# Kernel tuning notes

Measured on AMD Instinct MI355X. Metric: run time of the kernel, lower is better.

Reference implementation:

```python
import jax, jax.numpy as jnp
import numpy as np

B, NP, NM, C, H = 4, 256, 128, 128, 128
EPS = 1e-5

def layernorm(x, g, b):
    mu = jnp.mean(x, axis=-1, keepdims=True)
    var = jnp.var(x, axis=-1, keepdims=True)
    return (x - mu) * jax.lax.rsqrt(var + EPS) * g + b

def setup_inputs() -> dict:
    key = jax.random.key(0)
    ks = jax.random.split(key, 16)
    s = lambda d: 1.0 / np.sqrt(d)
    return {
        "z": jax.random.normal(ks[0], (B, NP, NM, C), jnp.float32),
        "z_mask": jnp.ones((B, NP, NM), jnp.float32),
        "pocket_pair": jax.random.normal(ks[1], (B, NP, NP, C), jnp.float32),
        "mol_pair": jax.random.normal(ks[2], (B, NM, NM, C), jnp.float32),
        "ln_g": jnp.ones((C,), jnp.float32), "ln_b": jnp.zeros((C,), jnp.float32),
        "lnh_g": jnp.ones((H,), jnp.float32), "lnh_b": jnp.zeros((H,), jnp.float32),
        "gw1": jax.random.uniform(ks[3], (C, H), jnp.float32, -s(C), s(C)),
        "gb1": jnp.zeros((H,), jnp.float32),
        "gw2": jax.random.uniform(ks[4], (C, H), jnp.float32, -s(C), s(C)),
        "gb2": jnp.zeros((H,), jnp.float32),
        "w1": jax.random.uniform(ks[5], (C, H), jnp.float32, -s(C), s(C)),
        "b1": jnp.zeros((H,), jnp.float32),
        "w2": jax.random.uniform(ks[6], (C, H), jnp.float32, -s(C), s(C)),
        "b2": jnp.zeros((H,), jnp.float32),
        "egw": jax.random.uniform(ks[7], (C, C), jnp.float32, -s(C), s(C)),
        "egb": jnp.zeros((C,), jnp.float32),
        "asw": jax.random.uniform(ks[8], (H, C), jnp.float32, -s(H), s(H)),
        "asb": jnp.zeros((C,), jnp.float32),
    }

def reference(z, z_mask, pocket_pair, mol_pair, ln_g, ln_b, lnh_g, lnh_b,
              gw1, gb1, gw2, gb2, w1, b1, w2, b2, egw, egb, asw, asb):
    m = z_mask[..., None]                      # [b,Np,Nm,1]
    zn = layernorm(z, ln_g, ln_b)              # [b,Np,Nm,C]
    pp = layernorm(pocket_pair, ln_g, ln_b)    # [b,Np,Np,C]
    mp = layernorm(mol_pair, ln_g, ln_b)       # [b,Nm,Nm,C]
    gate1 = lambda x: jax.nn.sigmoid(x @ gw1 + gb1) * (x @ w1 + b1)
    gate2 = lambda x: jax.nn.sigmoid(x @ gw2 + gb2) * (x @ w2 + b2)
    ab1 = gate1(zn) * m                        # [b,Np,Nm,H]
    ab2 = gate2(zn) * m                        # [b,Np,Nm,H]
    ppg = gate2(pp)                            # [b,Np,Np,H]
    mpg = gate1(mp)                            # [b,Nm,Nm,H]
    block1 = jnp.einsum('bikc,bkjc->bijc', ppg, ab1)   # [b,Np,Nm,H]
    block2 = jnp.einsum('bikc,bjkc->bijc', ab2, mpg)   # [b,Np,Nm,H]
    h = layernorm(block1 + block2, lnh_g, lnh_b)
    out = jax.nn.sigmoid(zn @ egw + egb) * (h @ asw + asb) * m
    return out
```

## Files before the change

kernel.cpp:

```cpp
#include <hip/hip_runtime.h>
#include <hip/hip_bf16.h>

#define DEVFN __device__ __forceinline__
using bf16 = __hip_bfloat16;
typedef __attribute__((ext_vector_type(8))) short short8;
typedef __attribute__((ext_vector_type(4))) float f32x4;
typedef __attribute__((ext_vector_type(4))) unsigned short us4;

constexpr int BB = 4, NP = 256, NM = 128, CC = 128, HH = 128;
constexpr float EPS = 1e-5f;

#define MFMA16(a,b,c) __builtin_amdgcn_mfma_f32_16x16x32_bf16((a),(b),(c),0,0,0)

DEVFN unsigned short bfbits(float v){ union{ bf16 b; unsigned short s; } u; u.b = __float2bfloat16(v); return u.s; }
DEVFN float bits2f(unsigned short s){ union{ unsigned int i; float f; } u; u.i = ((unsigned)s) << 16; return u.f; }
DEVFN float sigm(float x){ return 1.0f / (1.0f + __expf(-x)); }

__global__ __launch_bounds__(256)
void prep_weights_kernel(const float* __restrict__ gw1, const float* __restrict__ w1,
                         const float* __restrict__ gw2, const float* __restrict__ w2,
                         const float* __restrict__ egw, const float* __restrict__ asw,
                         bf16* __restrict__ wt)
{
  __shared__ float wl[128][129];
  const int bx = blockIdx.x;
  const float* W = (bx==0)?gw1 : (bx==1)?w1 : (bx==2)?gw2 : (bx==3)?w2 : (bx==4)?egw : asw;
  const int t = threadIdx.x;
  for (int i = 0; i < 16; ++i){
    int idx = t + 256*i;
    int k = idx >> 5, n0 = (idx & 31) * 4;
    float4 v = *reinterpret_cast<const float4*>(W + k*128 + n0);
    wl[k][n0] = v.x; wl[k][n0+1] = v.y; wl[k][n0+2] = v.z; wl[k][n0+3] = v.w;
  }
  __syncthreads();
  short* o = reinterpret_cast<short*>(wt) + bx * 16384;
  const int n = t >> 1, kh = t & 1;
  #pragma unroll
  for (int j = 0; j < 8; ++j){
    short8 p;
    #pragma unroll
    for (int u = 0; u < 8; ++u) p[u] = (short)bfbits(wl[kh*64 + j*8 + u][n]);
    *reinterpret_cast<short8*>(o + n*128 + kh*64 + j*8) = p;
  }
}

struct GateSmem {
  short xs[64*128];
  float lgb[2][128];
  float mk[64];
};

DEVFN void gate_pass64(const char* xb, const float* mk, int t, long obase, long R,
                       const short* wtg, const short* wtl,
                       const float* __restrict__ bgp, const float* __restrict__ blp,
                       bf16* outp)
{
  const int l = t & 63, w = t >> 6, lr = l & 15, lg = l >> 4;
  const int n0 = w * 32;
  short8 bgf[2][4], blf[2][4];
  #pragma unroll
  for (int nt = 0; nt < 2; ++nt)
    #pragma unroll
    for (int ks = 0; ks < 4; ++ks){
      int n = n0 + nt*16 + lr, ko = ks*32 + lg*8;
      bgf[nt][ks] = *reinterpret_cast<const short8*>(wtg + n*128 + ko);
      blf[nt][ks] = *reinterpret_cast<const short8*>(wtl + n*128 + ko);
    }
  float bgv[2] = { bgp[n0 + lr], bgp[n0 + 16 + lr] };
  float blv[2] = { blp[n0 + lr], blp[n0 + 16 + lr] };
  unsigned short* ob = reinterpret_cast<unsigned short*>(outp);

  #pragma unroll
  for (int mt = 0; mt < 4; ++mt){
    f32x4 zv = {0.f,0.f,0.f,0.f};
    f32x4 ag0 = zv, ag1 = zv, al0 = zv, al1 = zv;
    #pragma unroll
    for (int ks = 0; ks < 4; ++ks){
      int m = mt*16 + lr, ko = ks*32 + lg*8;
      short8 a = *reinterpret_cast<const short8*>(xb + ((m*256 + ko*2) ^ ((m & 7) << 4)));
      ag0 = MFMA16(a, bgf[0][ks], ag0);
      al0 = MFMA16(a, blf[0][ks], al0);
      ag1 = MFMA16(a, bgf[1][ks], ag1);
      al1 = MFMA16(a, blf[1][ks], al1);
    }
    #pragma unroll
    for (int nt = 0; nt < 2; ++nt){
      f32x4 ag = nt ? ag1 : ag0, al = nt ? al1 : al0;
      int h = n0 + nt*16 + lr;
      us4 pk;
      #pragma unroll
      for (int rg = 0; rg < 4; ++rg){
        int rowl = mt*16 + lg*4 + rg;
        float val = sigm(ag[rg] + bgv[nt]) * (al[rg] + blv[nt]) * mk[rowl];
        pk[rg] = bfbits(val);
      }
      *reinterpret_cast<us4*>(ob + obase + (long)h*R + mt*16 + lg*4) = pk;
    }
  }
}

DEVFN void eg_pass64(const char* xb, int t, long obase, long R,
                     const short* wtg, const float* __restrict__ bgp, bf16* outp)
{
  const int l = t & 63, w = t >> 6, lr = l & 15, lg = l >> 4;
  const int n0 = w * 32;
  short8 bgf[2][4];
  #pragma unroll
  for (int nt = 0; nt < 2; ++nt)
    #pragma unroll
    for (int ks = 0; ks < 4; ++ks){
      int n = n0 + nt*16 + lr, ko = ks*32 + lg*8;
      bgf[nt][ks] = *reinterpret_cast<const short8*>(wtg + n*128 + ko);
    }
  float bgv[2] = { bgp[n0 + lr], bgp[n0 + 16 + lr] };
  unsigned short* ob = reinterpret_cast<unsigned short*>(outp);

  #pragma unroll
  for (int mt = 0; mt < 4; ++mt){
    f32x4 zv = {0.f,0.f,0.f,0.f};
    f32x4 ag0 = zv, ag1 = zv;
    #pragma unroll
    for (int ks = 0; ks < 4; ++ks){
      int m = mt*16 + lr, ko = ks*32 + lg*8;
      short8 a = *reinterpret_cast<const short8*>(xb + ((m*256 + ko*2) ^ ((m & 7) << 4)));
      ag0 = MFMA16(a, bgf[0][ks], ag0);
      ag1 = MFMA16(a, bgf[1][ks], ag1);
    }
    #pragma unroll
    for (int nt = 0; nt < 2; ++nt){
      f32x4 ag = nt ? ag1 : ag0;
      int h = n0 + nt*16 + lr;
      us4 pk;
      #pragma unroll
      for (int rg = 0; rg < 4; ++rg) pk[rg] = bfbits(sigm(ag[rg] + bgv[nt]));
      *reinterpret_cast<us4*>(ob + obase + (long)h*R + mt*16 + lg*4) = pk;
    }
  }
}

constexpr int NZB = (BB*NP*NM)/64;
constexpr int NPB = (BB*NP*NP)/64;
constexpr int NMB = (BB*NM*NM)/64;

__global__ __launch_bounds__(256, 3)
void gate_all_kernel(const float* __restrict__ z, const float* __restrict__ zmask,
                     const float* __restrict__ pp, const float* __restrict__ mp,
                     const float* __restrict__ lng, const float* __restrict__ lnb,
                     const bf16* __restrict__ wt,
                     const float* __restrict__ gb1, const float* __restrict__ b1,
                     const float* __restrict__ gb2, const float* __restrict__ b2,
                     const float* __restrict__ egbv,
                     bf16* ab1, bf16* ab2, bf16* egp, bf16* ppg, bf16* mpg)
{
  __shared__ GateSmem sm;
  const int t = threadIdx.x;
  const short* wts = reinterpret_cast<const short*>(wt);

  int bx = blockIdx.x;
  const float* x; const float* mask = nullptr;
  long R; int npass = 1;
  const short *w1g, *w1l; const float *bg1v, *bl1v; bf16* o1;
  if (bx < NZB){
    x = z; mask = zmask; R = (long)NP*NM; npass = 3;
    w1g = wts + 0*16384; w1l = wts + 1*16384; bg1v = gb1; bl1v = b1; o1 = ab1;
  } else if (bx < NZB + NPB){
    bx -= NZB; x = pp; R = (long)NP*NP;
    w1g = wts + 2*16384; w1l = wts + 3*16384; bg1v = gb2; bl1v = b2; o1 = ppg;
  } else {
    bx -= NZB + NPB; x = mp; R = (long)NM*NM;
    w1g = wts + 0*16384; w1l = wts + 1*16384; bg1v = gb1; bl1v = b1; o1 = mpg;
  }
  const long row0 = (long)bx * 64;
  const int b = (int)(row0 / R);
  const long rowb = row0 - (long)b * R;
  const long obase = (long)b * 128 * R + rowb;

  if (t < 128){ sm.lgb[0][t] = lng[t]; sm.lgb[1][t] = lnb[t]; }
  if (t < 64) sm.mk[t] = mask ? mask[row0 + t] : 1.0f;

  const int r = t >> 2, hf = t & 3;
  const float4* xrow = reinterpret_cast<const float4*>(x + (row0 + r)*128 + hf*32);
  float4 vb[8];
  float s = 0.f, ss = 0.f;
  #pragma unroll
  for (int i = 0; i < 8; ++i){
    float4 v = xrow[i]; vb[i] = v;
    s  += v.x + v.y + v.z + v.w;
    ss += v.x*v.x + v.y*v.y + v.z*v.z + v.w*v.w;
  }
  s += __shfl_xor(s, 1);  ss += __shfl_xor(ss, 1);
  s += __shfl_xor(s, 2);  ss += __shfl_xor(ss, 2);
  const float mu = s * (1.f/128.f);
  const float rsg = rsqrtf(ss * (1.f/128.f) - mu*mu + EPS);
  __syncthreads();
  {
    char* xb = reinterpret_cast<char*>(sm.xs);
    #pragma unroll
    for (int j = 0; j < 4; ++j){
      float4 a = vb[2*j], c2 = vb[2*j+1];
      float vv[8] = {a.x, a.y, a.z, a.w, c2.x, c2.y, c2.z, c2.w};
      short8 p;
      #pragma unroll
      for (int u = 0; u < 8; ++u){
        int ch = hf*32 + j*8 + u;
        p[u] = (short)bfbits((vv[u] - mu) * rsg * sm.lgb[0][ch] + sm.lgb[1][ch]);
      }
      *reinterpret_cast<short8*>(xb + ((r*256 + hf*64 + j*16) ^ ((r & 7) << 4))) = p;
    }
  }
  __syncthreads();

  const char* xb = reinterpret_cast<const char*>(sm.xs);
  gate_pass64(xb, sm.mk, t, obase, R, w1g, w1l, bg1v, bl1v, o1);
  if (npass == 3){
    gate_pass64(xb, sm.mk, t, obase, R, wts + 2*16384, wts + 3*16384, gb2, b2, ab2);
    eg_pass64(xb, t, obase, R, wts + 4*16384, egbv, egp);
  }
}

DEVFN int b1swz(int j){ return (((j & 7) ^ ((j >> 3) & 7)) << 4); }

__global__ __launch_bounds__(256, 2)
void einsum_mfma_kernel(const bf16* __restrict__ ppg, const bf16* __restrict__ ab1,
                        const bf16* __restrict__ ab2, const bf16* __restrict__ mpg,
                        bf16* __restrict__ bsum)
{
  __shared__ short b1t[128*256];
  const int t = threadIdx.x, l = t & 63, w = t >> 6, lr = l & 15, lg = l >> 4;
  const int bc = blockIdx.x;
  const short* A1 = reinterpret_cast<const short*>(ppg) + (long)bc * (NP*NP);
  const short* B1 = reinterpret_cast<const short*>(ab1) + (long)bc * (NP*NM);
  const short* A2 = reinterpret_cast<const short*>(ab2) + (long)bc * (NP*NM);
  const short* B2 = reinterpret_cast<const short*>(mpg) + (long)bc * (NM*NM);

  char* lb = reinterpret_cast<char*>(b1t);
  for (int it = 0; it < 16; ++it){
    int idx = t + 256*it;
    int k = idx >> 4, j0 = (idx & 15) * 8;
    short8 v = *reinterpret_cast<const short8*>(B1 + idx*8);
    #pragma unroll
    for (int u = 0; u < 8; ++u){
      int j = j0 + u;
      *reinterpret_cast<short*>(lb + ((j*512 + k*2) ^ b1swz(j))) = v[u];
    }
  }
  __syncthreads();

  f32x4 zv = {0.f,0.f,0.f,0.f};
  f32x4 acc[4][8];
  #pragma unroll
  for (int i = 0; i < 4; ++i)
    #pragma unroll
    for (int j = 0; j < 8; ++j) acc[i][j] = zv;

  const int m0 = w * 64;
  for (int ks = 0; ks < 8; ++ks){
    int ko = ks*32 + lg*8;
    short8 af[4];
    #pragma unroll
    for (int mt = 0; mt < 4; ++mt)
      af[mt] = *reinterpret_cast<const short8*>(A1 + (m0 + mt*16 + lr)*256 + ko);
    short8 bf[8];
    #pragma unroll
    for (int nt = 0; nt < 8; ++nt){
      int n = nt*16 + lr;
      bf[nt] = *reinterpret_cast<const short8*>(lb + ((n*512 + ko*2) ^ b1swz(n)));
    }
    #pragma unroll
    for (int mt = 0; mt < 4; ++mt)
      #pragma unroll
      for (int nt = 0; nt < 8; ++nt)
        acc[mt][nt] = MFMA16(af[mt], bf[nt], acc[mt][nt]);
  }
  for (int ks = 0; ks < 4; ++ks){
    int ko = ks*32 + lg*8;
    short8 af[4];
    #pragma unroll
    for (int mt = 0; mt < 4; ++mt)
      af[mt] = *reinterpret_cast<const short8*>(A2 + (m0 + mt*16 + lr)*128 + ko);
    short8 bf[8];
    #pragma unroll
    for (int nt = 0; nt < 8; ++nt)
      bf[nt] = *reinterpret_cast<const short8*>(B2 + (nt*16 + lr)*128 + ko);
    #pragma unroll
    for (int mt = 0; mt < 4; ++mt)
      #pragma unroll
      for (int nt = 0; nt < 8; ++nt)
        acc[mt][nt] = MFMA16(af[mt], bf[nt], acc[mt][nt]);
  }
  unsigned short* out = reinterpret_cast<unsigned short*>(bsum) + (long)bc * (NP*NM);
  #pragma unroll
  for (int mt = 0; mt < 4; ++mt)
    #pragma unroll
    for (int nt = 0; nt < 8; ++nt)
      #pragma unroll
      for (int rg = 0; rg < 4; ++rg)
        out[(m0 + mt*16 + lg*4 + rg)*128 + nt*16 + lr] = bfbits(acc[mt][nt][rg]);
}

__global__ __launch_bounds__(256, 2)
void final_mfma_kernel(const bf16* __restrict__ bsum, const bf16* __restrict__ eg,
                       const float* __restrict__ mask,
                       const float* __restrict__ lnhg, const float* __restrict__ lnhb,
                       const bf16* __restrict__ wt, const float* __restrict__ asb,
                       float* __restrict__ out)
{
  __shared__ struct {
    short xsT[128][72];
    short xs[64*128];
    float lgb[2][128];
    float ps[4][64], pss[4][64];
    float mu[64], rs[64], mk[64];
  } sm;
  const int t = threadIdx.x, l = t & 63, w = t >> 6, lr = l & 15, lg = l >> 4;
  const long row0 = (long)blockIdx.x * 64;
  const int b = (int)(row0 >> 15);
  const long rowb = row0 & 32767;

  if (t < 128){ sm.lgb[0][t] = lnhg[t]; sm.lgb[1][t] = lnhb[t]; }
  if (t < 64) sm.mk[t] = mask[row0 + t];

  const short* bs = reinterpret_cast<const short*>(bsum);
  #pragma unroll
  for (int i = 0; i < 4; ++i){
    int idx = t + 256*i;
    int c = idx >> 3, j8 = idx & 7;
    short8 v = *reinterpret_cast<const short8*>(bs + (long)(b*128 + c)*32768 + rowb + j8*8);
    *reinterpret_cast<short8*>(&sm.xsT[c][j8*8]) = v;
  }
  __syncthreads();
  {
    int ij = t & 63, q = t >> 6;
    float s = 0.f, ss = 0.f;
    #pragma unroll
    for (int k = 0; k < 32; ++k){
      float v = bits2f((unsigned short)sm.xsT[q*32 + k][ij]);
      s += v; ss += v*v;
    }
    sm.ps[q][ij] = s; sm.pss[q][ij] = ss;
  }
  __syncthreads();
  if (t < 64){
    float s  = sm.ps[0][t] + sm.ps[1][t] + sm.ps[2][t] + sm.ps[3][t];
    float ss = sm.pss[0][t] + sm.pss[1][t] + sm.pss[2][t] + sm.pss[3][t];
    float mu = s * (1.f/128.f);
    float var = ss * (1.f/128.f) - mu*mu;
    sm.mu[t] = mu; sm.rs[t] = rsqrtf(var + EPS);
  }
  __syncthreads();
  {
    int ij = t & 63, q = t >> 6;
    float mu = sm.mu[ij], rg2 = sm.rs[ij];
    char* xb = reinterpret_cast<char*>(sm.xs);
    #pragma unroll
    for (int u = 0; u < 4; ++u){
      short8 p;
      #pragma unroll
      for (int e = 0; e < 8; ++e){
        int c = q*32 + u*8 + e;
        float v = bits2f((unsigned short)sm.xsT[c][ij]);
        p[e] = (short)bfbits((v - mu) * rg2 * sm.lgb[0][c] + sm.lgb[1][c]);
      }
      *reinterpret_cast<short8*>(xb + ((ij*256 + q*64 + u*16) ^ ((ij & 7) << 4))) = p;
    }
  }
  __syncthreads();

  const short* aswt = reinterpret_cast<const short*>(wt) + 5*16384;
  f32x4 zv = {0.f,0.f,0.f,0.f};
  f32x4 acc[8];
  #pragma unroll
  for (int i = 0; i < 8; ++i) acc[i] = zv;
  const char* xb = reinterpret_cast<const char*>(sm.xs);
  #pragma unroll
  for (int ks = 0; ks < 4; ++ks){
    int m = w*16 + lr, ko = ks*32 + lg*8;
    short8 a = *reinterpret_cast<const short8*>(xb + ((m*256 + ko*2) ^ ((m & 7) << 4)));
    #pragma unroll
    for (int nt = 0; nt < 8; ++nt){
      short8 bfr = *reinterpret_cast<const short8*>(aswt + (nt*16 + lr)*128 + ko);
      acc[nt] = MFMA16(a, bfr, acc[nt]);
    }
  }
  const unsigned short* egb2 = reinterpret_cast<const unsigned short*>(eg);
  #pragma unroll
  for (int nt = 0; nt < 8; ++nt){
    int co = nt*16 + lr;
    float bias = asb[co];
    us4 egv = *reinterpret_cast<const us4*>(egb2 + (long)(b*128 + co)*32768 + rowb + w*16 + lg*4);
    #pragma unroll
    for (int rg = 0; rg < 4; ++rg){
      int rowl = w*16 + lg*4 + rg;
      float val = bits2f(egv[rg]) * (acc[nt][rg] + bias) * sm.mk[rowl];
      out[(row0 + rowl)*128 + co] = val;
    }
  }
}

extern "C" void kernel_launch(void* const* d_in, const int* in_sizes, int n_in,
                              void* d_out, int out_size, void* d_ws, size_t ws_size,
                              hipStream_t stream)
{
  const float* z     = (const float*)d_in[0];
  const float* zmask = (const float*)d_in[1];
  const float* pp    = (const float*)d_in[2];
  const float* mp    = (const float*)d_in[3];
  const float* ln_g  = (const float*)d_in[4];
  const float* ln_b  = (const float*)d_in[5];
  const float* lnh_g = (const float*)d_in[6];
  const float* lnh_b = (const float*)d_in[7];
  const float* gw1   = (const float*)d_in[8];
  const float* gb1   = (const float*)d_in[9];
  const float* gw2   = (const float*)d_in[10];
  const float* gb2   = (const float*)d_in[11];
  const float* w1    = (const float*)d_in[12];
  const float* b1    = (const float*)d_in[13];
  const float* w2    = (const float*)d_in[14];
  const float* b2    = (const float*)d_in[15];
  const float* egw   = (const float*)d_in[16];
  const float* egb   = (const float*)d_in[17];
  const float* asw   = (const float*)d_in[18];
  const float* asb   = (const float*)d_in[19];
  float* out = (float*)d_out;

  const size_t ZE = (size_t)BB*NP*NM*HH;
  const size_t PE = (size_t)BB*NP*NP*HH;
  const size_t ME = (size_t)BB*NM*NM*HH;
  char* ws = (char*)d_ws;
  size_t off = 0;
  bf16* wt   = (bf16*)(ws + off); off += 6 * 16384 * 2;
  bf16* ab1  = (bf16*)(ws + off); off += ZE * 2;
  bf16* ab2  = (bf16*)(ws + off); off += ZE * 2;
  bf16* egp  = (bf16*)(ws + off); off += ZE * 2;
  bf16* ppg  = (bf16*)(ws + off); off += PE * 2;
  bf16* mpg  = (bf16*)(ws + off); off += ME * 2;
  bf16* bsum = (bf16*)(ws + off); off += ZE * 2;
  if (ws_size < off) return;

  prep_weights_kernel<<<6, 256, 0, stream>>>(gw1, w1, gw2, w2, egw, asw, wt);

  gate_all_kernel<<<NZB + NPB + NMB, 256, 0, stream>>>(
      z, zmask, pp, mp, ln_g, ln_b, wt,
      gb1, b1, gb2, b2, egb,
      ab1, ab2, egp, ppg, mpg);

  einsum_mfma_kernel<<<BB*CC, 256, 0, stream>>>(ppg, ab1, ab2, mpg, bsum);

  final_mfma_kernel<<<(BB*NP*NM)/64, 256, 0, stream>>>(
      bsum, egp, zmask, lnh_g, lnh_b, wt, asb, out);
}
```

Measured before the change: 306.2 us.

## Use 32x32 MFMA and 128-row tiles in gate projection kernel

The gate kernel now processes 128 rows per block instead of 64 and switches from 16x16x32 to 32x32x16 bf16 MFMA, so each wave owns 32 output channels across 32-row tiles. Loading weight fragments once per block over twice as many rows halves block count and weight reloads, and the larger MFMA needs fewer LDS A-fragment reads per flop. Costs are double the LDS tile, more registers per thread (16 float4 row values, f32x16 accumulators), which may hurt occupancy under launch_bounds(256,3).

```diff
diff --git a/kernel.cpp b/kernel.cpp
--- a/kernel.cpp
+++ b/kernel.cpp
@@ -5,12 +5,14 @@
 using bf16 = __hip_bfloat16;
 typedef __attribute__((ext_vector_type(8))) short short8;
 typedef __attribute__((ext_vector_type(4))) float f32x4;
+typedef __attribute__((ext_vector_type(16))) float f32x16;
 typedef __attribute__((ext_vector_type(4))) unsigned short us4;
 
 constexpr int BB = 4, NP = 256, NM = 128, CC = 128, HH = 128;
 constexpr float EPS = 1e-5f;
 
 #define MFMA16(a,b,c) __builtin_amdgcn_mfma_f32_16x16x32_bf16((a),(b),(c),0,0,0)
+#define MFMA32(a,b,c) __builtin_amdgcn_mfma_f32_32x32x16_bf16((a),(b),(c),0,0,0)
 
 DEVFN unsigned short bfbits(float v){ union{ bf16 b; unsigned short s; } u; u.b = __float2bfloat16(v); return u.s; }
 DEVFN float bits2f(unsigned short s){ union{ unsigned int i; float f; } u; u.i = ((unsigned)s) << 16; return u.f; }
@@ -45,102 +47,98 @@
 }
 
 struct GateSmem {
-  short xs[64*128];
+  short xs[128*128];
   float lgb[2][128];
-  float mk[64];
+  float mk[128];
 };
 
-DEVFN void gate_pass64(const char* xb, const float* mk, int t, long obase, long R,
+DEVFN void gate32_pass(const char* xb, const float* mk, int t, long obase, long R,
                        const short* wtg, const short* wtl,
                        const float* __restrict__ bgp, const float* __restrict__ blp,
                        bf16* outp)
 {
-  const int l = t & 63, w = t >> 6, lr = l & 15, lg = l >> 4;
-  const int n0 = w * 32;
-  short8 bgf[2][4], blf[2][4];
-  #pragma unroll
-  for (int nt = 0; nt < 2; ++nt)
-    #pragma unroll
-    for (int ks = 0; ks < 4; ++ks){
-      int n = n0 + nt*16 + lr, ko = ks*32 + lg*8;
-      bgf[nt][ks] = *reinterpret_cast<const short8*>(wtg + n*128 + ko);
-      blf[nt][ks] = *reinterpret_cast<const short8*>(wtl + n*128 + ko);
-    }
-  float bgv[2] = { bgp[n0 + lr], bgp[n0 + 16 + lr] };
-  float blv[2] = { blp[n0 + lr], blp[n0 + 16 + lr] };
+  const int l = t & 63, w = t >> 6;
+  const int cn = l & 31, kh = l >> 5;
+  const int h = w * 32 + cn;
+  short8 bg8[8], bl8[8];
+  #pragma unroll
+  for (int ks = 0; ks < 8; ++ks){
+    int ko = ks*16 + kh*8;
+    bg8[ks] = *reinterpret_cast<const short8*>(wtg + h*128 + ko);
+    bl8[ks] = *reinterpret_cast<const short8*>(wtl + h*128 + ko);
+  }
+  const float bgv = bgp[h], blv = blp[h];
   unsigned short* ob = reinterpret_cast<unsigned short*>(outp);
+  const long hbase = obase + (long)h * R;
 
   #pragma unroll
   for (int mt = 0; mt < 4; ++mt){
-    f32x4 zv = {0.f,0.f,0.f,0.f};
-    f32x4 ag0 = zv, ag1 = zv, al0 = zv, al1 = zv;
-    #pragma unroll
-    for (int ks = 0; ks < 4; ++ks){
-      int m = mt*16 + lr, ko = ks*32 + lg*8;
-      short8 a = *reinterpret_cast<const short8*>(xb + ((m*256 + ko*2) ^ ((m & 7) << 4)));
-      ag0 = MFMA16(a, bgf[0][ks], ag0);
-      al0 = MFMA16(a, blf[0][ks], al0);
-      ag1 = MFMA16(a, bgf[1][ks], ag1);
-      al1 = MFMA16(a, blf[1][ks], al1);
-    }
-    #pragma unroll
-    for (int nt = 0; nt < 2; ++nt){
-      f32x4 ag = nt ? ag1 : ag0, al = nt ? al1 : al0;
-      int h = n0 + nt*16 + lr;
+    f32x16 accg, accl;
+    #pragma unroll
+    for (int i = 0; i < 16; ++i){ accg[i] = 0.f; accl[i] = 0.f; }
+    #pragma unroll
+    for (int ks = 0; ks < 8; ++ks){
+      int m = mt*32 + cn;
+      int kb = (ks*16 + kh*8) * 2;
+      short8 a = *reinterpret_cast<const short8*>(xb + ((m*256 + kb) ^ ((m & 7) << 4)));
+      accg = MFMA32(a, bg8[ks], accg);
+      accl = MFMA32(a, bl8[ks], accl);
+    }
+    #pragma unroll
+    for (int q = 0; q < 4; ++q){
+      int rbase = mt*32 + q*8 + kh*4;
       us4 pk;
       #pragma unroll
       for (int rg = 0; rg < 4; ++rg){
-        int rowl = mt*16 + lg*4 + rg;
-        float val = sigm(ag[rg] + bgv[nt]) * (al[rg] + blv[nt]) * mk[rowl];
-        pk[rg] = bfbits(val);
+        float gg = accg[q*4+rg] + bgv;
+        float ll = accl[q*4+rg] + blv;
+        pk[rg] = bfbits(sigm(gg) * ll * mk[rbase + rg]);
       }
-      *reinterpret_cast<us4*>(ob + obase + (long)h*R + mt*16 + lg*4) = pk;
-    }
-  }
-}
-
-DEVFN void eg_pass64(const char* xb, int t, long obase, long R,
+      *reinterpret_cast<us4*>(ob + hbase + rbase) = pk;
+    }
+  }
+}
+
+DEVFN void eg32_pass(const char* xb, int t, long obase, long R,
                      const short* wtg, const float* __restrict__ bgp, bf16* outp)
 {
-  const int l = t & 63, w = t >> 6, lr = l & 15, lg = l >> 4;
-  const int n0 = w * 32;
-  short8 bgf[2][4];
-  #pragma unroll
-  for (int nt = 0; nt < 2; ++nt)
-    #pragma unroll
-    for (int ks = 0; ks < 4; ++ks){
-      int n = n0 + nt*16 + lr, ko = ks*32 + lg*8;
-      bgf[nt][ks] = *reinterpret_cast<const short8*>(wtg + n*128 + ko);
-    }
-  float bgv[2] = { bgp[n0 + lr], bgp[n0 + 16 + lr] };
+  const int l = t & 63, w = t >> 6;
+  const int cn = l & 31, kh = l >> 5;
+  const int h = w * 32 + cn;
+  short8 bg8[8];
+  #pragma unroll
+  for (int ks = 0; ks < 8; ++ks)
+    bg8[ks] = *reinterpret_cast<const short8*>(wtg + h*128 + ks*16 + kh*8);
+  const float bgv = bgp[h];
   unsigned short* ob = reinterpret_cast<unsigned short*>(outp);
+  const long hbase = obase + (long)h * R;
 
   #pragma unroll
   for (int mt = 0; mt < 4; ++mt){
-    f32x4 zv = {0.f,0.f,0.f,0.f};
-    f32x4 ag0 = zv, ag1 = zv;
-    #pragma unroll
-    for (int ks = 0; ks < 4; ++ks){
-      int m = mt*16 + lr, ko = ks*32 + lg*8;
-      short8 a = *reinterpret_cast<const short8*>(xb + ((m*256 + ko*2) ^ ((m & 7) << 4)));
-      ag0 = MFMA16(a, bgf[0][ks], ag0);
-      ag1 = MFMA16(a, bgf[1][ks], ag1);
-    }
-    #pragma unroll
-    for (int nt = 0; nt < 2; ++nt){
-      f32x4 ag = nt ? ag1 : ag0;
-      int h = n0 + nt*16 + lr;
+    f32x16 accg;
+    #pragma unroll
+    for (int i = 0; i < 16; ++i) accg[i] = 0.f;
+    #pragma unroll
+    for (int ks = 0; ks < 8; ++ks){
+      int m = mt*32 + cn;
+      int kb = (ks*16 + kh*8) * 2;
+      short8 a = *reinterpret_cast<const short8*>(xb + ((m*256 + kb) ^ ((m & 7) << 4)));
+      accg = MFMA32(a, bg8[ks], accg);
+    }
+    #pragma unroll
+    for (int q = 0; q < 4; ++q){
+      int rbase = mt*32 + q*8 + kh*4;
       us4 pk;
       #pragma unroll
-      for (int rg = 0; rg < 4; ++rg) pk[rg] = bfbits(sigm(ag[rg] + bgv[nt]));
-      *reinterpret_cast<us4*>(ob + obase + (long)h*R + mt*16 + lg*4) = pk;
-    }
-  }
-}
-
-constexpr int NZB = (BB*NP*NM)/64;
-constexpr int NPB = (BB*NP*NP)/64;
-constexpr int NMB = (BB*NM*NM)/64;
+      for (int rg = 0; rg < 4; ++rg) pk[rg] = bfbits(sigm(accg[q*4+rg] + bgv));
+      *reinterpret_cast<us4*>(ob + hbase + rbase) = pk;
+    }
+  }
+}
+
+constexpr int NZB = (BB*NP*NM)/128;
+constexpr int NPB = (BB*NP*NP)/128;
+constexpr int NMB = (BB*NM*NM)/128;
 
 __global__ __launch_bounds__(256, 3)
 void gate_all_kernel(const float* __restrict__ z, const float* __restrict__ zmask,
@@ -170,51 +168,54 @@
     bx -= NZB + NPB; x = mp; R = (long)NM*NM;
     w1g = wts + 0*16384; w1l = wts + 1*16384; bg1v = gb1; bl1v = b1; o1 = mpg;
   }
-  const long row0 = (long)bx * 64;
+  const long row0 = (long)bx * 128;
   const int b = (int)(row0 / R);
   const long rowb = row0 - (long)b * R;
   const long obase = (long)b * 128 * R + rowb;
 
-  if (t < 128){ sm.lgb[0][t] = lng[t]; sm.lgb[1][t] = lnb[t]; }
-  if (t < 64) sm.mk[t] = mask ? mask[row0 + t] : 1.0f;
-
-  const int r = t >> 2, hf = t & 3;
-  const float4* xrow = reinterpret_cast<const float4*>(x + (row0 + r)*128 + hf*32);
-  float4 vb[8];
+  if (t < 128){
+    sm.lgb[0][t] = lng[t];
+    sm.lgb[1][t] = lnb[t];
+    sm.mk[t] = mask ? mask[row0 + t] : 1.0f;
+  }
+
+  const int r = t >> 1, hf = t & 1;
+  const float4* xrow = reinterpret_cast<const float4*>(x + (row0 + r)*128 + hf*64);
+  float4 vb[16];
   float s = 0.f, ss = 0.f;
   #pragma unroll
-  for (int i = 0; i < 8; ++i){
+  for (int i = 0; i < 16; ++i){
     float4 v = xrow[i]; vb[i] = v;
     s  += v.x + v.y + v.z + v.w;
     ss += v.x*v.x + v.y*v.y + v.z*v.z + v.w*v.w;
   }
-  s += __shfl_xor(s, 1);  ss += __shfl_xor(ss, 1);
-  s += __shfl_xor(s, 2);  ss += __shfl_xor(ss, 2);
+  s  += __shfl_xor(s, 1);
+  ss += __shfl_xor(ss, 1);
   const float mu = s * (1.f/128.f);
   const float rsg = rsqrtf(ss * (1.f/128.f) - mu*mu + EPS);
   __syncthreads();
   {
-    char* xb = reinterpret_cast<char*>(sm.xs);
-    #pragma unroll
-    for (int j = 0; j < 4; ++j){
+    char* xbw = reinterpret_cast<char*>(sm.xs);
+    #pragma unroll
+    for (int j = 0; j < 8; ++j){
       float4 a = vb[2*j], c2 = vb[2*j+1];
       float vv[8] = {a.x, a.y, a.z, a.w, c2.x, c2.y, c2.z, c2.w};
       short8 p;
       #pragma unroll
       for (int u = 0; u < 8; ++u){
-        int ch = hf*32 + j*8 + u;
+        int ch = hf*64 + j*8 + u;
         p[u] = (short)bfbits((vv[u] - mu) * rsg * sm.lgb[0][ch] + sm.lgb[1][ch]);
       }
-      *reinterpret_cast<short8*>(xb + ((r*256 + hf*64 + j*16) ^ ((r & 7) << 4))) = p;
+      *reinterpret_cast<short8*>(xbw + ((r*256 + hf*128 + j*16) ^ ((r & 7) << 4))) = p;
     }
   }
   __syncthreads();
 
   const char* xb = reinterpret_cast<const char*>(sm.xs);
-  gate_pass64(xb, sm.mk, t, obase, R, w1g, w1l, bg1v, bl1v, o1);
+  gate32_pass(xb, sm.mk, t, obase, R, w1g, w1l, bg1v, bl1v, o1);
   if (npass == 3){
-    gate_pass64(xb, sm.mk, t, obase, R, wts + 2*16384, wts + 3*16384, gb2, b2, ab2);
-    eg_pass64(xb, t, obase, R, wts + 4*16384, egbv, egp);
+    gate32_pass(xb, sm.mk, t, obase, R, wts + 2*16384, wts + 3*16384, gb2, b2, ab2);
+    eg32_pass(xb, t, obase, R, wts + 4*16384, egbv, egp);
   }
 }
 
@@ -351,7 +352,7 @@
   {
     int ij = t & 63, q = t >> 6;
     float mu = sm.mu[ij], rg2 = sm.rs[ij];
-    char* xb = reinterpret_cast<char*>(sm.xs);
+    char* xbw = reinterpret_cast<char*>(sm.xs);
     #pragma unroll
     for (int u = 0; u < 4; ++u){
       short8 p;
@@ -361,7 +362,7 @@
         float v = bits2f((unsigned short)sm.xsT[c][ij]);
         p[e] = (short)bfbits((v - mu) * rg2 * sm.lgb[0][c] + sm.lgb[1][c]);
       }
-      *reinterpret_cast<short8*>(xb + ((ij*256 + q*64 + u*16) ^ ((ij & 7) << 4))) = p;
+      *reinterpret_cast<short8*>(xbw + ((ij*256 + q*64 + u*16) ^ ((ij & 7) << 4))) = p;
     }
   }
   __syncthreads();
```

Result: slower. 373.2 us (+21.9%).
